# Optimization experiments

Measured on AMD Instinct MI355X. Metric: run time of the kernel, lower is better.

## Reference

```python
import jax, jax.numpy as jnp
import numpy as np

S, B, F, H = 256, 16, 200, 100


def setup_inputs() -> dict:
    key = jax.random.key(0)
    k1, k2, k3, k4, k5, k6 = jax.random.split(key, 6)
    inp = {}
    inp["input"] = jax.random.normal(k1, (S, B, F), dtype=jnp.float32)
    inp["sequence_lengths"] = jax.random.randint(k2, (B,), 1, S + 1, dtype=jnp.int32)
    sf, sh = 1.0 / np.sqrt(F), 1.0 / np.sqrt(H)
    inp["Wq"] = jax.random.normal(k3, (F, H), dtype=jnp.float32) * sf
    inp["Wk"] = jax.random.normal(k4, (F, H), dtype=jnp.float32) * sf
    inp["b"] = jax.random.normal(k5, (H,), dtype=jnp.float32) * sh
    inp["v"] = jax.random.normal(k6, (H,), dtype=jnp.float32) * sh
    return inp


def reference(input, sequence_lengths, Wq, Wk, b, v):
    # input: (S, B, F); sequence_lengths: (B,)
    q = jnp.einsum('sbf,fh->sbh', input, Wq)  # (S, B, H)
    k = jnp.einsum('sbf,fh->sbh', input, Wk)  # (S, B, H)
    # Additive attention scores e[t, s, b] = v . tanh(Wq x_t + Wk x_s + b)
    e = jnp.einsum('tsbh,h->tsb', jnp.tanh(q[:, None] + k[None, :] + b), v)  # (Sq, Sk, B)
    valid = jnp.arange(S)[:, None] < sequence_lengths[None, :]  # (S, B), True where in-sequence
    e = jnp.where(valid[None, :, :], e, -jnp.inf)  # mask keys beyond each length
    a = jax.nn.softmax(e, axis=1)  # softmax over keys
    attended = jnp.einsum('tsb,sbf->tbf', a, input)  # value = input (transform=False)
    # Fused masked-segment concat-pool over valid timesteps of each sequence
    m = valid[:, :, None]
    lengths = sequence_lengths.astype(attended.dtype)[:, None]
    mean_pool = jnp.sum(jnp.where(m, attended, 0.0), axis=0) / lengths  # (B, F)
    max_pool = jnp.max(jnp.where(m, attended, -jnp.inf), axis=0)        # (B, F)
    return jnp.concatenate([max_pool, mean_pool], axis=-1)  # (B, 2F)
```

## Files before the change

### kernel.cpp

```cpp
#include <hip/hip_runtime.h>
#include <math.h>

#define S_DIM 256
#define B_DIM 16
#define F_DIM 200
#define H_DIM 100
#define ROWS (S_DIM * B_DIM)

__global__ __launch_bounds__(256) void k1_proj_exp(
    const float* __restrict__ input, const float* __restrict__ Wq,
    const float* __restrict__ Wk, const float* __restrict__ bias,
    float* __restrict__ Eq, float* __restrict__ Ek)
{
    __shared__ float pq[8][128], pk[8][128];
    const int tid = threadIdx.x;
    const int h = tid & 127;
    const int fg = tid >> 7;
    const int hh = (h < H_DIM) ? h : (H_DIM - 1);
    const int r0 = blockIdx.x * 8;
    float accq[8], acck[8];
#pragma unroll
    for (int r = 0; r < 8; ++r) { accq[r] = 0.f; acck[r] = 0.f; }
    const int fb = fg * 100;
    for (int f4 = 0; f4 < 25; ++f4) {
        const int f = fb + f4 * 4;
        const float wq0 = Wq[(f + 0) * H_DIM + hh];
        const float wq1 = Wq[(f + 1) * H_DIM + hh];
        const float wq2 = Wq[(f + 2) * H_DIM + hh];
        const float wq3 = Wq[(f + 3) * H_DIM + hh];
        const float wk0 = Wk[(f + 0) * H_DIM + hh];
        const float wk1 = Wk[(f + 1) * H_DIM + hh];
        const float wk2 = Wk[(f + 2) * H_DIM + hh];
        const float wk3 = Wk[(f + 3) * H_DIM + hh];
#pragma unroll
        for (int r = 0; r < 8; ++r) {
            const float4 xv = *(const float4*)&input[(r0 + r) * F_DIM + f];
            accq[r] = fmaf(xv.x, wq0, accq[r]);
            accq[r] = fmaf(xv.y, wq1, accq[r]);
            accq[r] = fmaf(xv.z, wq2, accq[r]);
            accq[r] = fmaf(xv.w, wq3, accq[r]);
            acck[r] = fmaf(xv.x, wk0, acck[r]);
            acck[r] = fmaf(xv.y, wk1, acck[r]);
            acck[r] = fmaf(xv.z, wk2, acck[r]);
            acck[r] = fmaf(xv.w, wk3, acck[r]);
        }
    }
    if (fg) {
#pragma unroll
        for (int r = 0; r < 8; ++r) { pq[r][h] = accq[r]; pk[r][h] = acck[r]; }
    }
    __syncthreads();
    if (!fg && h < H_DIM) {
        const float bv = bias[h];
#pragma unroll
        for (int r = 0; r < 8; ++r) {
            const float q = accq[r] + pq[r][h];
            const float k = acck[r] + pk[r][h] + bv;
            Eq[(r0 + r) * H_DIM + h] = __expf(2.f * q);
            Ek[(r0 + r) * H_DIM + h] = __expf(2.f * k);
        }
    }
}

__global__ __launch_bounds__(256) void k2_scores(
    const float* __restrict__ Eq, const float* __restrict__ Ek,
    const float* __restrict__ vvec, const int* __restrict__ seqlen,
    float* __restrict__ p)
{
    __shared__ float4 klds[64 * 27];
    const int tid = threadIdx.x;
    const int b = blockIdx.z;
    const int len = seqlen[b];
    const int s0 = blockIdx.y * 64;
    const int t0 = blockIdx.x * 8;
    if (s0 >= len || t0 >= len) return;
    const float4* Ek4 = (const float4*)Ek;
    for (int idx = tid; idx < 64 * 25; idx += 256) {
        int r = idx / 25, c = idx - r * 25;
        klds[r * 27 + c] = Ek4[((s0 + r) * B_DIM + b) * 25 + c];
    }
    __syncthreads();
    const int s = tid & 63;
    const int th = __builtin_amdgcn_readfirstlane(tid >> 6);
    const int tbase = t0 + th * 2;
    const int ni = len - tbase;
    if (ni <= 0) return;

    float sv = 0.f;
    for (int h4 = 0; h4 < 25; ++h4) {
        const float4 vv = *(const float4*)&vvec[h4 * 4];
        sv += (vv.x + vv.y) + (vv.z + vv.w);
    }
    float acc0 = sv, acc1 = sv;
    const float* eq0 = Eq + ((tbase + 0) * B_DIM + b) * H_DIM;
    const float* eq1 = Eq + ((tbase + 1) * B_DIM + b) * H_DIM;
    for (int h4 = 0; h4 < 25; ++h4) {
        const float4 kk = klds[s * 27 + h4];
        const float4 vv = *(const float4*)&vvec[h4 * 4];
        const float4 q0 = *(const float4*)(eq0 + h4 * 4);
        const float4 q1 = *(const float4*)(eq1 + h4 * 4);
        const float m2x = -2.f * vv.x, m2y = -2.f * vv.y;
        const float m2z = -2.f * vv.z, m2w = -2.f * vv.w;
        acc0 = fmaf(m2x, __builtin_amdgcn_rcpf(fmaf(q0.x, kk.x, 1.f)), acc0);
        acc0 = fmaf(m2y, __builtin_amdgcn_rcpf(fmaf(q0.y, kk.y, 1.f)), acc0);
        acc0 = fmaf(m2z, __builtin_amdgcn_rcpf(fmaf(q0.z, kk.z, 1.f)), acc0);
        acc0 = fmaf(m2w, __builtin_amdgcn_rcpf(fmaf(q0.w, kk.w, 1.f)), acc0);
        acc1 = fmaf(m2x, __builtin_amdgcn_rcpf(fmaf(q1.x, kk.x, 1.f)), acc1);
        acc1 = fmaf(m2y, __builtin_amdgcn_rcpf(fmaf(q1.y, kk.y, 1.f)), acc1);
        acc1 = fmaf(m2z, __builtin_amdgcn_rcpf(fmaf(q1.z, kk.z, 1.f)), acc1);
        acc1 = fmaf(m2w, __builtin_amdgcn_rcpf(fmaf(q1.w, kk.w, 1.f)), acc1);
    }
    const int ss = s0 + s;
    if (ss < len) {
        p[((tbase + 0) * B_DIM + b) * S_DIM + ss] = __expf(acc0);
        if (ni > 1) p[((tbase + 1) * B_DIM + b) * S_DIM + ss] = __expf(acc1);
    }
}

__global__ __launch_bounds__(256) void k3_attend_pool(
    const float* __restrict__ p, const float* __restrict__ input,
    const int* __restrict__ seqlen, float* __restrict__ out)
{
    __shared__ float lm[4][8], ls[4][8];
    const int tid = threadIdx.x;
    const int b = blockIdx.y;
    const int f0 = blockIdx.x * 8;
    const int len = seqlen[b];
    const int tg = tid >> 6, lane = tid & 63;
    const int t = tg * 64 + lane;
    float mx[8], sm[8];
#pragma unroll
    for (int j = 0; j < 8; ++j) { mx[j] = -INFINITY; sm[j] = 0.f; }

    if (tg * 64 < len) {
        float acc[8];
#pragma unroll
        for (int j = 0; j < 8; ++j) acc[j] = 0.f;
        float psum = 0.f;
        const float* prow = p + (t * B_DIM + b) * S_DIM;
        int s = 0;
        for (; s + 4 <= len; s += 4) {
            const float4 pv = *(const float4*)(prow + s);
            const float pvals[4] = {pv.x, pv.y, pv.z, pv.w};
            psum += (pv.x + pv.y) + (pv.z + pv.w);
#pragma unroll
            for (int q = 0; q < 4; ++q) {
                const float* xrow = &input[((s + q) * B_DIM + b) * F_DIM + f0];
                const float4 xa = *(const float4*)xrow;
                const float4 xb = *(const float4*)(xrow + 4);
                acc[0] = fmaf(pvals[q], xa.x, acc[0]);
                acc[1] = fmaf(pvals[q], xa.y, acc[1]);
                acc[2] = fmaf(pvals[q], xa.z, acc[2]);
                acc[3] = fmaf(pvals[q], xa.w, acc[3]);
                acc[4] = fmaf(pvals[q], xb.x, acc[4]);
                acc[5] = fmaf(pvals[q], xb.y, acc[5]);
                acc[6] = fmaf(pvals[q], xb.z, acc[6]);
                acc[7] = fmaf(pvals[q], xb.w, acc[7]);
            }
        }
        for (; s < len; ++s) {
            const float pvv = prow[s];
            const float* xrow = &input[(s * B_DIM + b) * F_DIM + f0];
            const float4 xa = *(const float4*)xrow;
            const float4 xb = *(const float4*)(xrow + 4);
            psum += pvv;
            acc[0] = fmaf(pvv, xa.x, acc[0]);
            acc[1] = fmaf(pvv, xa.y, acc[1]);
            acc[2] = fmaf(pvv, xa.z, acc[2]);
            acc[3] = fmaf(pvv, xa.w, acc[3]);
            acc[4] = fmaf(pvv, xb.x, acc[4]);
            acc[5] = fmaf(pvv, xb.y, acc[5]);
            acc[6] = fmaf(pvv, xb.z, acc[6]);
            acc[7] = fmaf(pvv, xb.w, acc[7]);
        }
        const float rs = 1.f / psum;
        const bool tv = (t < len);
#pragma unroll
        for (int j = 0; j < 8; ++j) {
            const float a = acc[j] * rs;
            mx[j] = tv ? a : -INFINITY;
            sm[j] = tv ? a : 0.f;
        }
    }
#pragma unroll
    for (int j = 0; j < 8; ++j) {
        float m = mx[j], s2 = sm[j];
        for (int off = 32; off; off >>= 1) {
            m = fmaxf(m, __shfl_xor(m, off));
            s2 += __shfl_xor(s2, off);
        }
        if (lane == 0) { lm[tg][j] = m; ls[tg][j] = s2; }
    }
    __syncthreads();
    if (tid < 8) {
        float m = lm[0][tid], s2 = ls[0][tid];
#pragma unroll
        for (int g = 1; g < 4; ++g) { m = fmaxf(m, lm[g][tid]); s2 += ls[g][tid]; }
        out[b * (2 * F_DIM) + f0 + tid] = m;
        out[b * (2 * F_DIM) + F_DIM + f0 + tid] = s2 / (float)len;
    }
}

extern "C" void kernel_launch(void* const* d_in, const int* in_sizes, int n_in,
                              void* d_out, int out_size, void* d_ws, size_t ws_size,
                              hipStream_t stream)
{
    const float* input  = (const float*)d_in[0];
    const int*   seqlen = (const int*)d_in[1];
    const float* Wq     = (const float*)d_in[2];
    const float* Wk     = (const float*)d_in[3];
    const float* bias   = (const float*)d_in[4];
    const float* vvec   = (const float*)d_in[5];
    float* out = (float*)d_out;

    float* ws = (float*)d_ws;
    float* Eq = ws;
    float* Ek = ws + 409600;
    float* p  = ws + 819200;

    k1_proj_exp<<<ROWS / 8, 256, 0, stream>>>(input, Wq, Wk, bias, Eq, Ek);
    k2_scores<<<dim3(S_DIM / 8, S_DIM / 64, B_DIM), 256, 0, stream>>>(Eq, Ek, vvec, seqlen, p);
    k3_attend_pool<<<dim3(F_DIM / 8, B_DIM), 256, 0, stream>>>(p, input, seqlen, out);
}
```

Measured before the change: 121.9 us.

## Split attend and pool into separate kernels, move softmax sums into scores kernel

The score kernel now pairs tanh terms so one reciprocal covers two h elements. It also reduces each block's exp values into per-block partial row sums. The old attend+pool kernel (only 25x16 blocks, each looping over all queries and keys) is replaced by an attend kernel over query tiles and features, writing attended values to workspace. A small pool kernel then normalizes by the summed partials and does max/mean pooling. This trades a workspace round trip and an extra launch for much more parallelism in the attend stage, and the paired reciprocal risks overflow when the product of denominators gets large.

```diff
diff --git a/kernel.cpp b/kernel.cpp
--- a/kernel.cpp
+++ b/kernel.cpp
@@ -65,7 +65,7 @@
 __global__ __launch_bounds__(256) void k2_scores(
     const float* __restrict__ Eq, const float* __restrict__ Ek,
     const float* __restrict__ vvec, const int* __restrict__ seqlen,
-    float* __restrict__ p)
+    float* __restrict__ p, float* __restrict__ psum4)
 {
     __shared__ float4 klds[64 * 27];
     const int tid = threadIdx.x;
@@ -99,105 +99,123 @@
         const float4 vv = *(const float4*)&vvec[h4 * 4];
         const float4 q0 = *(const float4*)(eq0 + h4 * 4);
         const float4 q1 = *(const float4*)(eq1 + h4 * 4);
-        const float m2x = -2.f * vv.x, m2y = -2.f * vv.y;
-        const float m2z = -2.f * vv.z, m2w = -2.f * vv.w;
-        acc0 = fmaf(m2x, __builtin_amdgcn_rcpf(fmaf(q0.x, kk.x, 1.f)), acc0);
-        acc0 = fmaf(m2y, __builtin_amdgcn_rcpf(fmaf(q0.y, kk.y, 1.f)), acc0);
-        acc0 = fmaf(m2z, __builtin_amdgcn_rcpf(fmaf(q0.z, kk.z, 1.f)), acc0);
-        acc0 = fmaf(m2w, __builtin_amdgcn_rcpf(fmaf(q0.w, kk.w, 1.f)), acc0);
-        acc1 = fmaf(m2x, __builtin_amdgcn_rcpf(fmaf(q1.x, kk.x, 1.f)), acc1);
-        acc1 = fmaf(m2y, __builtin_amdgcn_rcpf(fmaf(q1.y, kk.y, 1.f)), acc1);
-        acc1 = fmaf(m2z, __builtin_amdgcn_rcpf(fmaf(q1.z, kk.z, 1.f)), acc1);
-        acc1 = fmaf(m2w, __builtin_amdgcn_rcpf(fmaf(q1.w, kk.w, 1.f)), acc1);
+        const float vmx = -2.f * vv.x, vmy = -2.f * vv.y;
+        const float vmz = -2.f * vv.z, vmw = -2.f * vv.w;
+        {
+            float dx = fmaf(q0.x, kk.x, 1.f), dy = fmaf(q0.y, kk.y, 1.f);
+            float N = fmaf(vmx, dy, vmy * dx);
+            acc0 = fmaf(N, __builtin_amdgcn_rcpf(dx * dy), acc0);
+            float dz = fmaf(q0.z, kk.z, 1.f), dw = fmaf(q0.w, kk.w, 1.f);
+            float M = fmaf(vmz, dw, vmw * dz);
+            acc0 = fmaf(M, __builtin_amdgcn_rcpf(dz * dw), acc0);
+        }
+        {
+            float dx = fmaf(q1.x, kk.x, 1.f), dy = fmaf(q1.y, kk.y, 1.f);
+            float N = fmaf(vmx, dy, vmy * dx);
+            acc1 = fmaf(N, __builtin_amdgcn_rcpf(dx * dy), acc1);
+            float dz = fmaf(q1.z, kk.z, 1.f), dw = fmaf(q1.w, kk.w, 1.f);
+            float M = fmaf(vmz, dw, vmw * dz);
+            acc1 = fmaf(M, __builtin_amdgcn_rcpf(dz * dw), acc1);
+        }
     }
     const int ss = s0 + s;
+    float pe0 = 0.f, pe1 = 0.f;
     if (ss < len) {
-        p[((tbase + 0) * B_DIM + b) * S_DIM + ss] = __expf(acc0);
-        if (ni > 1) p[((tbase + 1) * B_DIM + b) * S_DIM + ss] = __expf(acc1);
-    }
-}
-
-__global__ __launch_bounds__(256) void k3_attend_pool(
+        pe0 = __expf(acc0);
+        p[((tbase + 0) * B_DIM + b) * S_DIM + ss] = pe0;
+        if (ni > 1) {
+            pe1 = __expf(acc1);
+            p[((tbase + 1) * B_DIM + b) * S_DIM + ss] = pe1;
+        }
+    }
+    for (int off = 32; off; off >>= 1) {
+        pe0 += __shfl_xor(pe0, off);
+        pe1 += __shfl_xor(pe1, off);
+    }
+    if (s == 0) {
+        float* pp = psum4 + (blockIdx.y * S_DIM + tbase) * B_DIM + b;
+        pp[0] = pe0;
+        if (ni > 1) pp[B_DIM] = pe1;
+    }
+}
+
+__global__ __launch_bounds__(256) void k3_attend(
     const float* __restrict__ p, const float* __restrict__ input,
+    const int* __restrict__ seqlen, float* __restrict__ att)
+{
+    const int tid = threadIdx.x;
+    const int b = blockIdx.y;
+    const int len = seqlen[b];
+    const int t0 = blockIdx.x * 16;
+    if (t0 >= len) return;
+    const int f = (tid < F_DIM) ? tid : (F_DIM - 1);
+    float acc[16];
+#pragma unroll
+    for (int i = 0; i < 16; ++i) acc[i] = 0.f;
+    const float* pb = p + b * S_DIM;
+    int s = 0;
+    for (; s + 4 <= len; s += 4) {
+        const float x0 = input[((s + 0) * B_DIM + b) * F_DIM + f];
+        const float x1 = input[((s + 1) * B_DIM + b) * F_DIM + f];
+        const float x2 = input[((s + 2) * B_DIM + b) * F_DIM + f];
+        const float x3 = input[((s + 3) * B_DIM + b) * F_DIM + f];
+#pragma unroll
+        for (int i = 0; i < 16; ++i) {
+            const float4 pv = *(const float4*)&pb[(t0 + i) * B_DIM * S_DIM + s];
+            acc[i] = fmaf(pv.x, x0, acc[i]);
+            acc[i] = fmaf(pv.y, x1, acc[i]);
+            acc[i] = fmaf(pv.z, x2, acc[i]);
+            acc[i] = fmaf(pv.w, x3, acc[i]);
+        }
+    }
+    for (; s < len; ++s) {
+        const float xv = input[(s * B_DIM + b) * F_DIM + f];
+#pragma unroll
+        for (int i = 0; i < 16; ++i)
+            acc[i] = fmaf(pb[(t0 + i) * B_DIM * S_DIM + s], xv, acc[i]);
+    }
+    if (tid < F_DIM) {
+#pragma unroll
+        for (int i = 0; i < 16; ++i)
+            att[((t0 + i) * B_DIM + b) * F_DIM + tid] = acc[i];
+    }
+}
+
+__global__ __launch_bounds__(1024) void k4_pool(
+    const float* __restrict__ att, const float* __restrict__ psum4,
     const int* __restrict__ seqlen, float* __restrict__ out)
 {
-    __shared__ float lm[4][8], ls[4][8];
-    const int tid = threadIdx.x;
-    const int b = blockIdx.y;
-    const int f0 = blockIdx.x * 8;
+    __shared__ float smx[4][256];
+    __shared__ float ssm[4][256];
+    const int b = blockIdx.x;
+    const int tid = threadIdx.x;
+    const int f = tid & 255;
+    const int q = tid >> 8;
     const int len = seqlen[b];
-    const int tg = tid >> 6, lane = tid & 63;
-    const int t = tg * 64 + lane;
-    float mx[8], sm[8];
-#pragma unroll
-    for (int j = 0; j < 8; ++j) { mx[j] = -INFINITY; sm[j] = 0.f; }
-
-    if (tg * 64 < len) {
-        float acc[8];
-#pragma unroll
-        for (int j = 0; j < 8; ++j) acc[j] = 0.f;
-        float psum = 0.f;
-        const float* prow = p + (t * B_DIM + b) * S_DIM;
-        int s = 0;
-        for (; s + 4 <= len; s += 4) {
-            const float4 pv = *(const float4*)(prow + s);
-            const float pvals[4] = {pv.x, pv.y, pv.z, pv.w};
-            psum += (pv.x + pv.y) + (pv.z + pv.w);
-#pragma unroll
-            for (int q = 0; q < 4; ++q) {
-                const float* xrow = &input[((s + q) * B_DIM + b) * F_DIM + f0];
-                const float4 xa = *(const float4*)xrow;
-                const float4 xb = *(const float4*)(xrow + 4);
-                acc[0] = fmaf(pvals[q], xa.x, acc[0]);
-                acc[1] = fmaf(pvals[q], xa.y, acc[1]);
-                acc[2] = fmaf(pvals[q], xa.z, acc[2]);
-                acc[3] = fmaf(pvals[q], xa.w, acc[3]);
-                acc[4] = fmaf(pvals[q], xb.x, acc[4]);
-                acc[5] = fmaf(pvals[q], xb.y, acc[5]);
-                acc[6] = fmaf(pvals[q], xb.z, acc[6]);
-                acc[7] = fmaf(pvals[q], xb.w, acc[7]);
-            }
-        }
-        for (; s < len; ++s) {
-            const float pvv = prow[s];
-            const float* xrow = &input[(s * B_DIM + b) * F_DIM + f0];
-            const float4 xa = *(const float4*)xrow;
-            const float4 xb = *(const float4*)(xrow + 4);
-            psum += pvv;
-            acc[0] = fmaf(pvv, xa.x, acc[0]);
-            acc[1] = fmaf(pvv, xa.y, acc[1]);
-            acc[2] = fmaf(pvv, xa.z, acc[2]);
-            acc[3] = fmaf(pvv, xa.w, acc[3]);
-            acc[4] = fmaf(pvv, xb.x, acc[4]);
-            acc[5] = fmaf(pvv, xb.y, acc[5]);
-            acc[6] = fmaf(pvv, xb.z, acc[6]);
-            acc[7] = fmaf(pvv, xb.w, acc[7]);
-        }
-        const float rs = 1.f / psum;
-        const bool tv = (t < len);
-#pragma unroll
-        for (int j = 0; j < 8; ++j) {
-            const float a = acc[j] * rs;
-            mx[j] = tv ? a : -INFINITY;
-            sm[j] = tv ? a : 0.f;
-        }
-    }
-#pragma unroll
-    for (int j = 0; j < 8; ++j) {
-        float m = mx[j], s2 = sm[j];
-        for (int off = 32; off; off >>= 1) {
-            m = fmaxf(m, __shfl_xor(m, off));
-            s2 += __shfl_xor(s2, off);
-        }
-        if (lane == 0) { lm[tg][j] = m; ls[tg][j] = s2; }
-    }
+    const int nsy = (len + 63) >> 6;
+    float mx = -INFINITY, sm = 0.f;
+    if (f < F_DIM) {
+        for (int t = q; t < len; t += 4) {
+            float ps = psum4[t * B_DIM + b];
+            for (int sy = 1; sy < nsy; ++sy)
+                ps += psum4[(sy * S_DIM + t) * B_DIM + b];
+            const float a = att[(t * B_DIM + b) * F_DIM + f] *
+                            __builtin_amdgcn_rcpf(ps);
+            mx = fmaxf(mx, a);
+            sm += a;
+        }
+    }
+    smx[q][f] = mx;
+    ssm[q][f] = sm;
     __syncthreads();
-    if (tid < 8) {
-        float m = lm[0][tid], s2 = ls[0][tid];
-#pragma unroll
-        for (int g = 1; g < 4; ++g) { m = fmaxf(m, lm[g][tid]); s2 += ls[g][tid]; }
-        out[b * (2 * F_DIM) + f0 + tid] = m;
-        out[b * (2 * F_DIM) + F_DIM + f0 + tid] = s2 / (float)len;
+    if (q == 0 && f < F_DIM) {
+#pragma unroll
+        for (int k = 1; k < 4; ++k) {
+            mx = fmaxf(mx, smx[k][f]);
+            sm += ssm[k][f];
+        }
+        out[b * (2 * F_DIM) + f] = mx;
+        out[b * (2 * F_DIM) + F_DIM + f] = sm / (float)len;
     }
 }
 
@@ -214,11 +232,14 @@
     float* out = (float*)d_out;
 
     float* ws = (float*)d_ws;
-    float* Eq = ws;
-    float* Ek = ws + 409600;
-    float* p  = ws + 819200;
+    float* Eq    = ws;
+    float* Ek    = ws + 409600;
+    float* p     = ws + 819200;
+    float* psum4 = ws + 819200 + 1048576;
+    float* att   = ws;
 
     k1_proj_exp<<<ROWS / 8, 256, 0, stream>>>(input, Wq, Wk, bias, Eq, Ek);
-    k2_scores<<<dim3(S_DIM / 8, S_DIM / 64, B_DIM), 256, 0, stream>>>(Eq, Ek, vvec, seqlen, p);
-    k3_attend_pool<<<dim3(F_DIM / 8, B_DIM), 256, 0, stream>>>(p, input, seqlen, out);
-}
+    k2_scores<<<dim3(S_DIM / 8, S_DIM / 64, B_DIM), 256, 0, stream>>>(Eq, Ek, vvec, seqlen, p, psum4);
+    k3_attend<<<dim3(S_DIM / 16, B_DIM), 256, 0, stream>>>(p, input, seqlen, att);
+    k4_pool<<<B_DIM, 1024, 0, stream>>>(att, psum4, seqlen, out);
+}
```

Measured after the change: 219.4 us. 1.8x slower.

## Transpose score matrix layout, stage input in LDS, pair reciprocals in score kernel

Applied to the files above, without the earlier changes.

The score kernel now stores p as [b][s][t] through an LDS transpose tile, so the attend kernel reads p coalesced across t for each key s. The attend kernel stages its 8-feature input slice for all timesteps in LDS instead of re-reading it from global memory per thread. The score kernel also merges two rcp calls into one by combining fractions, which cuts transcendental work but adds multiplies and some overflow risk from the product of the exp terms. Threads with t beyond len now compute instead of exiting early, and the attend kernel no longer skips invalid t groups, so some work that was skipped before is now done.

```diff
diff --git a/kernel.cpp b/kernel.cpp
--- a/kernel.cpp
+++ b/kernel.cpp
@@ -68,6 +68,7 @@
     float* __restrict__ p)
 {
     __shared__ float4 klds[64 * 27];
+    __shared__ float pt[64][9];
     const int tid = threadIdx.x;
     const int b = blockIdx.z;
     const int len = seqlen[b];
@@ -81,10 +82,8 @@
     }
     __syncthreads();
     const int s = tid & 63;
-    const int th = __builtin_amdgcn_readfirstlane(tid >> 6);
+    const int th = tid >> 6;
     const int tbase = t0 + th * 2;
-    const int ni = len - tbase;
-    if (ni <= 0) return;
 
     float sv = 0.f;
     for (int h4 = 0; h4 < 25; ++h4) {
@@ -99,21 +98,33 @@
         const float4 vv = *(const float4*)&vvec[h4 * 4];
         const float4 q0 = *(const float4*)(eq0 + h4 * 4);
         const float4 q1 = *(const float4*)(eq1 + h4 * 4);
-        const float m2x = -2.f * vv.x, m2y = -2.f * vv.y;
-        const float m2z = -2.f * vv.z, m2w = -2.f * vv.w;
-        acc0 = fmaf(m2x, __builtin_amdgcn_rcpf(fmaf(q0.x, kk.x, 1.f)), acc0);
-        acc0 = fmaf(m2y, __builtin_amdgcn_rcpf(fmaf(q0.y, kk.y, 1.f)), acc0);
-        acc0 = fmaf(m2z, __builtin_amdgcn_rcpf(fmaf(q0.z, kk.z, 1.f)), acc0);
-        acc0 = fmaf(m2w, __builtin_amdgcn_rcpf(fmaf(q0.w, kk.w, 1.f)), acc0);
-        acc1 = fmaf(m2x, __builtin_amdgcn_rcpf(fmaf(q1.x, kk.x, 1.f)), acc1);
-        acc1 = fmaf(m2y, __builtin_amdgcn_rcpf(fmaf(q1.y, kk.y, 1.f)), acc1);
-        acc1 = fmaf(m2z, __builtin_amdgcn_rcpf(fmaf(q1.z, kk.z, 1.f)), acc1);
-        acc1 = fmaf(m2w, __builtin_amdgcn_rcpf(fmaf(q1.w, kk.w, 1.f)), acc1);
-    }
-    const int ss = s0 + s;
-    if (ss < len) {
-        p[((tbase + 0) * B_DIM + b) * S_DIM + ss] = __expf(acc0);
-        if (ni > 1) p[((tbase + 1) * B_DIM + b) * S_DIM + ss] = __expf(acc1);
+        const float vmx = -2.f * vv.x, vmy = -2.f * vv.y;
+        const float vmz = -2.f * vv.z, vmw = -2.f * vv.w;
+        {
+            float dx = fmaf(q0.x, kk.x, 1.f), dy = fmaf(q0.y, kk.y, 1.f);
+            float N = fmaf(vmx, dy, vmy * dx);
+            acc0 = fmaf(N, __builtin_amdgcn_rcpf(dx * dy), acc0);
+            float dz = fmaf(q0.z, kk.z, 1.f), dw = fmaf(q0.w, kk.w, 1.f);
+            float M = fmaf(vmz, dw, vmw * dz);
+            acc0 = fmaf(M, __builtin_amdgcn_rcpf(dz * dw), acc0);
+        }
+        {
+            float dx = fmaf(q1.x, kk.x, 1.f), dy = fmaf(q1.y, kk.y, 1.f);
+            float N = fmaf(vmx, dy, vmy * dx);
+            acc1 = fmaf(N, __builtin_amdgcn_rcpf(dx * dy), acc1);
+            float dz = fmaf(q1.z, kk.z, 1.f), dw = fmaf(q1.w, kk.w, 1.f);
+            float M = fmaf(vmz, dw, vmw * dz);
+            acc1 = fmaf(M, __builtin_amdgcn_rcpf(dz * dw), acc1);
+        }
+    }
+    pt[s][th * 2 + 0] = __expf(acc0);
+    pt[s][th * 2 + 1] = __expf(acc1);
+    __syncthreads();
+    float* pb = p + (b * S_DIM + s0) * S_DIM + t0;
+#pragma unroll
+    for (int v = tid; v < 512; v += 256) {
+        const int sr = v >> 3, tr = v & 7;
+        if (s0 + sr < len) pb[sr * S_DIM + tr] = pt[sr][tr];
     }
 }
 
@@ -121,81 +132,77 @@
     const float* __restrict__ p, const float* __restrict__ input,
     const int* __restrict__ seqlen, float* __restrict__ out)
 {
+    __shared__ float4 xlds4[512];
     __shared__ float lm[4][8], ls[4][8];
     const int tid = threadIdx.x;
     const int b = blockIdx.y;
-    const int f0 = blockIdx.x * 8;
     const int len = seqlen[b];
-    const int tg = tid >> 6, lane = tid & 63;
-    const int t = tg * 64 + lane;
-    float mx[8], sm[8];
-#pragma unroll
-    for (int j = 0; j < 8; ++j) { mx[j] = -INFINITY; sm[j] = 0.f; }
-
-    if (tg * 64 < len) {
-        float acc[8];
-#pragma unroll
-        for (int j = 0; j < 8; ++j) acc[j] = 0.f;
-        float psum = 0.f;
-        const float* prow = p + (t * B_DIM + b) * S_DIM;
-        int s = 0;
-        for (; s + 4 <= len; s += 4) {
-            const float4 pv = *(const float4*)(prow + s);
-            const float pvals[4] = {pv.x, pv.y, pv.z, pv.w};
-            psum += (pv.x + pv.y) + (pv.z + pv.w);
-#pragma unroll
-            for (int q = 0; q < 4; ++q) {
-                const float* xrow = &input[((s + q) * B_DIM + b) * F_DIM + f0];
-                const float4 xa = *(const float4*)xrow;
-                const float4 xb = *(const float4*)(xrow + 4);
-                acc[0] = fmaf(pvals[q], xa.x, acc[0]);
-                acc[1] = fmaf(pvals[q], xa.y, acc[1]);
-                acc[2] = fmaf(pvals[q], xa.z, acc[2]);
-                acc[3] = fmaf(pvals[q], xa.w, acc[3]);
-                acc[4] = fmaf(pvals[q], xb.x, acc[4]);
-                acc[5] = fmaf(pvals[q], xb.y, acc[5]);
-                acc[6] = fmaf(pvals[q], xb.z, acc[6]);
-                acc[7] = fmaf(pvals[q], xb.w, acc[7]);
-            }
-        }
-        for (; s < len; ++s) {
-            const float pvv = prow[s];
-            const float* xrow = &input[(s * B_DIM + b) * F_DIM + f0];
-            const float4 xa = *(const float4*)xrow;
-            const float4 xb = *(const float4*)(xrow + 4);
-            psum += pvv;
-            acc[0] = fmaf(pvv, xa.x, acc[0]);
-            acc[1] = fmaf(pvv, xa.y, acc[1]);
-            acc[2] = fmaf(pvv, xa.z, acc[2]);
-            acc[3] = fmaf(pvv, xa.w, acc[3]);
-            acc[4] = fmaf(pvv, xb.x, acc[4]);
-            acc[5] = fmaf(pvv, xb.y, acc[5]);
-            acc[6] = fmaf(pvv, xb.z, acc[6]);
-            acc[7] = fmaf(pvv, xb.w, acc[7]);
-        }
-        const float rs = 1.f / psum;
-        const bool tv = (t < len);
-#pragma unroll
-        for (int j = 0; j < 8; ++j) {
-            const float a = acc[j] * rs;
-            mx[j] = tv ? a : -INFINITY;
-            sm[j] = tv ? a : 0.f;
-        }
-    }
+    const int base = b * 50 + blockIdx.x * 2;
+    const float4* in4 = (const float4*)input;
+    for (int i = tid; i < 512; i += 256) {
+        const int s = i >> 1, half = i & 1;
+        xlds4[i] = in4[s * (B_DIM * 50) + base + half];
+    }
+    __syncthreads();
+
+    float acc[8];
+#pragma unroll
+    for (int j = 0; j < 8; ++j) acc[j] = 0.f;
+    float psum = 0.f;
+    const float* pb = p + b * (S_DIM * S_DIM) + tid;
+    int s = 0;
+    for (; s + 4 <= len; s += 4) {
+#pragma unroll
+        for (int q = 0; q < 4; ++q) {
+            const float pv = pb[(s + q) * S_DIM];
+            const float4 xa = xlds4[(s + q) * 2];
+            const float4 xb = xlds4[(s + q) * 2 + 1];
+            psum += pv;
+            acc[0] = fmaf(pv, xa.x, acc[0]);
+            acc[1] = fmaf(pv, xa.y, acc[1]);
+            acc[2] = fmaf(pv, xa.z, acc[2]);
+            acc[3] = fmaf(pv, xa.w, acc[3]);
+            acc[4] = fmaf(pv, xb.x, acc[4]);
+            acc[5] = fmaf(pv, xb.y, acc[5]);
+            acc[6] = fmaf(pv, xb.z, acc[6]);
+            acc[7] = fmaf(pv, xb.w, acc[7]);
+        }
+    }
+    for (; s < len; ++s) {
+        const float pv = pb[s * S_DIM];
+        const float4 xa = xlds4[s * 2];
+        const float4 xb = xlds4[s * 2 + 1];
+        psum += pv;
+        acc[0] = fmaf(pv, xa.x, acc[0]);
+        acc[1] = fmaf(pv, xa.y, acc[1]);
+        acc[2] = fmaf(pv, xa.z, acc[2]);
+        acc[3] = fmaf(pv, xa.w, acc[3]);
+        acc[4] = fmaf(pv, xb.x, acc[4]);
+        acc[5] = fmaf(pv, xb.y, acc[5]);
+        acc[6] = fmaf(pv, xb.z, acc[6]);
+        acc[7] = fmaf(pv, xb.w, acc[7]);
+    }
+
+    const float rp = __builtin_amdgcn_rcpf(psum);
+    const bool ok = (tid < len);
+    const int w = tid >> 6, lane = tid & 63;
 #pragma unroll
     for (int j = 0; j < 8; ++j) {
-        float m = mx[j], s2 = sm[j];
+        const float a = acc[j] * rp;
+        float m = ok ? a : -INFINITY;
+        float s2 = ok ? a : 0.f;
         for (int off = 32; off; off >>= 1) {
             m = fmaxf(m, __shfl_xor(m, off));
             s2 += __shfl_xor(s2, off);
         }
-        if (lane == 0) { lm[tg][j] = m; ls[tg][j] = s2; }
+        if (lane == 0) { lm[w][j] = m; ls[w][j] = s2; }
     }
     __syncthreads();
     if (tid < 8) {
         float m = lm[0][tid], s2 = ls[0][tid];
 #pragma unroll
         for (int g = 1; g < 4; ++g) { m = fmaxf(m, lm[g][tid]); s2 += ls[g][tid]; }
+        const int f0 = blockIdx.x * 8;
         out[b * (2 * F_DIM) + f0 + tid] = m;
         out[b * (2 * F_DIM) + F_DIM + f0 + tid] = s2 / (float)len;
     }
```

Measured after the change: 111.3 us. 1.09x faster.
